# Kernel tuning notes

Measured on AMD Instinct MI355X. Metric: run time of the kernel, lower is better.

The kernel has to match this reference:

```python
import jax, jax.numpy as jnp
import numpy as np

N, E = 50000, 200000
SIZES = [16, 32, 16]
EDIM = 8
EPS = 1e-5


def setup_inputs() -> dict:
    key = jax.random.key(0)
    ks = jax.random.split(key, 16)
    inp = {
        "x": jax.random.normal(ks[0], (N, SIZES[0]), jnp.float32),
        "edge_attr": jax.random.normal(ks[1], (E, EDIM), jnp.float32),
        "edge_index": jax.random.randint(ks[2], (2, E), 0, N, dtype=jnp.int32),
    }
    ki = 3
    for l in range(2):
        fin, fout = SIZES[l], SIZES[l + 1]
        m = fin * fout
        # xavier-ish init matching torch.nn.init.xavier_uniform_ scales
        inp[f"W1_{l}"] = jax.random.normal(ks[ki], (EDIM, m), jnp.float32) / np.float32(np.sqrt(EDIM)); ki += 1
        inp[f"b1_{l}"] = jnp.zeros((m,), jnp.float32)
        inp[f"W2_{l}"] = jax.random.normal(ks[ki], (m, m), jnp.float32) * np.float32(0.01 / np.sqrt(m)); ki += 1
        inp[f"b2_{l}"] = jnp.zeros((m,), jnp.float32)
        inp[f"root_{l}"] = jax.random.normal(ks[ki], (fin, fout), jnp.float32) / np.float32(np.sqrt(fin)); ki += 1
        inp[f"bias_{l}"] = jnp.zeros((fout,), jnp.float32)
        inp[f"gamma_{l}"] = jnp.ones((fout,), jnp.float32)
        inp[f"beta_{l}"] = jnp.zeros((fout,), jnp.float32)
    return inp


def _lrelu(v):
    return jnp.where(v >= 0, v, 0.01 * v)


def _nnconv(x, src, dst, edge_attr, W1, b1, W2, b2, root, bias, fin, fout):
    # edge MLP -> per-edge weight matrix [E, fin, fout]
    h = _lrelu(edge_attr @ W1 + b1) @ W2 + b2
    h = h.reshape(-1, fin, fout)
    # gather source node features, tiny per-edge matmul
    msg = jnp.einsum('ei,eio->eo', x[src], h)  # [E, fout]
    # scatter-mean aggregate at destination nodes
    agg = jax.ops.segment_sum(msg, dst, num_segments=N)
    deg = jax.ops.segment_sum(jnp.ones((msg.shape[0],), msg.dtype), dst, num_segments=N)
    agg = agg / jnp.maximum(deg, 1.0)[:, None]
    return agg + x @ root + bias


def _bn(v, gamma, beta):
    # BatchNorm1d (training mode: batch stats, biased variance)
    mu = v.mean(0)
    var = v.var(0)
    return (v - mu) * jax.lax.rsqrt(var + EPS) * gamma + beta


def reference(x, edge_attr,
              W1_0, b1_0, W2_0, b2_0, root_0, bias_0, gamma_0, beta_0,
              W1_1, b1_1, W2_1, b2_1, root_1, bias_1, gamma_1, beta_1,
              edge_index):
    src, dst = edge_index[0], edge_index[1]
    h = _nnconv(x, src, dst, edge_attr, W1_0, b1_0, W2_0, b2_0, root_0, bias_0, SIZES[0], SIZES[1])
    h = _lrelu(_bn(h, gamma_0, beta_0))
    h = _nnconv(h, src, dst, edge_attr, W1_1, b1_1, W2_1, b2_1, root_1, bias_1, SIZES[1], SIZES[2])
    return _bn(h, gamma_1, beta_1)
```

## Files before the change

### kernel.cpp

```cpp
#include <hip/hip_runtime.h>
#include <hip/hip_bf16.h>

typedef __attribute__((ext_vector_type(4))) float f32x4;
typedef __attribute__((ext_vector_type(8))) short s16x8;
typedef __attribute__((ext_vector_type(4))) int int4v;

#define DEVI __device__ __forceinline__

constexpr int NN = 50000;
constexpr int NE = 200000;
constexpr float BN_EPS = 1e-5f;

DEVI float bfbits2f(unsigned v) { union { unsigned u; float f; } t; t.u = v << 16; return t.f; }
DEVI float lrelu_f(float v) { return v >= 0.f ? v : 0.01f * v; }

__global__ void k_transpose_w2(const float* __restrict__ A0, const float* __restrict__ A1,
                               __hip_bfloat16* __restrict__ T0, __hip_bfloat16* __restrict__ T1) {
  const float* W2 = blockIdx.y ? A1 : A0;
  __hip_bfloat16* W2T = blockIdx.y ? T1 : T0;
  __shared__ float tile[32][33];
  int bx = blockIdx.x % 16, by = blockIdx.x / 16;
  int t = threadIdx.x;
  int r = t / 32, c = t % 32;
  for (int rr = r; rr < 32; rr += 8)
    tile[rr][c] = W2[(size_t)(by * 32 + rr) * 512 + bx * 32 + c];
  __syncthreads();
  for (int rr = r; rr < 32; rr += 8)
    W2T[(size_t)(bx * 32 + rr) * 512 + by * 32 + c] = __float2bfloat16(tile[c][rr]);
}

__global__ void k_transpose_w1(const float* __restrict__ A0, const float* __restrict__ A1,
                               __hip_bfloat16* __restrict__ T0, __hip_bfloat16* __restrict__ T1) {
  const float* W1 = blockIdx.y ? A1 : A0;
  __hip_bfloat16* W1T = blockIdx.y ? T1 : T0;
  int tid = blockIdx.x * 256 + threadIdx.x;
  if (tid < 8 * 512) {
    int k = tid / 512, n = tid % 512;
    W1T[n * 8 + k] = __float2bfloat16(W1[tid]);
  }
}

__global__ void k_count(const int* __restrict__ dst, int* __restrict__ cnt) {
  int e = blockIdx.x * 256 + threadIdx.x;
  if (e < NE) atomicAdd(&cnt[dst[e]], 1);
}

constexpr int SCAN_ELEMS = 1024;
__global__ void k_scan1(const int* __restrict__ cnt, int* __restrict__ base, int* __restrict__ aux, int n) {
  __shared__ int sw[256];
  int b = blockIdx.x, t = threadIdx.x;
  int i0 = b * SCAN_ELEMS + t * 4;
  int v[4]; int s = 0;
  #pragma unroll
  for (int j = 0; j < 4; j++) { int idx = i0 + j; v[j] = (idx < n) ? cnt[idx] : 0; s += v[j]; }
  sw[t] = s; __syncthreads();
  for (int d = 1; d < 256; d <<= 1) {
    int val = (t >= d) ? sw[t - d] : 0;
    __syncthreads();
    sw[t] += val;
    __syncthreads();
  }
  int run = (t > 0) ? sw[t - 1] : 0;
  #pragma unroll
  for (int j = 0; j < 4; j++) { int idx = i0 + j; if (idx < n) base[idx] = run; run += v[j]; }
  if (t == 255) aux[b] = sw[255];
}

__global__ void k_scan2(int* aux, int nb) {
  if (threadIdx.x == 0 && blockIdx.x == 0) {
    int run = 0;
    for (int i = 0; i < nb; i++) { int v = aux[i]; aux[i] = run; run += v; }
  }
}

__global__ void k_scan3(int* __restrict__ base, int* __restrict__ cursor, const int* __restrict__ aux, int n) {
  int i = blockIdx.x * 256 + threadIdx.x;
  if (i < n) { int v = base[i] + aux[i / SCAN_ELEMS]; base[i] = v; cursor[i] = v; }
}

__global__ void k_place(const int* __restrict__ dst, int* __restrict__ cursor, int* __restrict__ perm) {
  int e = blockIdx.x * 256 + threadIdx.x;
  if (e < NE) { int p = atomicAdd(&cursor[dst[e]], 1); perm[p] = e; }
}

template <int FIN, int FOUT>
__global__ __launch_bounds__(256, 2)
void k_edge(const float* __restrict__ x, const float* __restrict__ ea,
            const int* __restrict__ srcI,
            const __hip_bfloat16* __restrict__ W1T, const float* __restrict__ b1,
            const __hip_bfloat16* __restrict__ W2T, const float* __restrict__ b2,
            __hip_bfloat16* __restrict__ msgb)
{
  static_assert(FOUT == 32 || FOUT == 16, "");
  constexpr int TM = 256;
  constexpr int CG = 32;
  constexpr int NCGI = 16;
  constexpr int KH = 256;
  constexpr int NKC = 4;
  constexpr int NOT = FOUT / 16;
  constexpr int XLDS = TM + 8;

  __shared__ __align__(16) char bbuf[2][CG * 512];
  __shared__ __align__(16) char gbuf[4][4096];
  __shared__ __align__(16) __hip_bfloat16 xlt[FIN][XLDS];

  const int tid = threadIdx.x;
  const int lane = tid & 63, w = tid >> 6;
  const int l15 = lane & 15, l4 = lane >> 4;
  const int e0 = blockIdx.x * TM;
  const int rem = min(TM, NE - e0);
  const int wrow0 = w * 64;

  union { s16x8 v; int i4[4]; } earow;
  {
    int er = e0 + min(tid, rem - 1);
    float4 v0 = *(const float4*)(ea + (size_t)er * 8);
    float4 v1 = *(const float4*)(ea + (size_t)er * 8 + 4);
    __hip_bfloat16* p = (__hip_bfloat16*)&earow;
    p[0] = __float2bfloat16(v0.x); p[1] = __float2bfloat16(v0.y);
    p[2] = __float2bfloat16(v0.z); p[3] = __float2bfloat16(v0.w);
    p[4] = __float2bfloat16(v1.x); p[5] = __float2bfloat16(v1.y);
    p[6] = __float2bfloat16(v1.z); p[7] = __float2bfloat16(v1.w);
    int s = srcI[er];
    #pragma unroll
    for (int q = 0; q < FIN / 4; q++) {
      float4 xv4 = *(const float4*)(x + (size_t)s * FIN + q * 4);
      xlt[q * 4 + 0][tid] = __float2bfloat16(xv4.x);
      xlt[q * 4 + 1][tid] = __float2bfloat16(xv4.y);
      xlt[q * 4 + 2][tid] = __float2bfloat16(xv4.z);
      xlt[q * 4 + 3][tid] = __float2bfloat16(xv4.w);
    }
  }

  f32x4 msg[4][NOT];
  #pragma unroll
  for (int rt = 0; rt < 4; rt++)
    #pragma unroll
    for (int ot = 0; ot < NOT; ot++) msg[rt][ot] = (f32x4)(0.f);

  s16x8 af[NKC][4][2];
  const int st_col = tid >> 3, st_s = tid & 7;
  const char* W2Tb = (const char*)W2T;
  char* gme = gbuf[w];
  int4v sr[4];

  for (int sw = 0; sw < 2; ++sw) {
    {
      const char* gp = W2Tb + (size_t)st_col * 1024 + sw * 512;
      #pragma unroll
      for (int j = 0; j < 4; j++) sr[j] = *(const int4v*)(gp + st_s * 16 + j * 128);
    }
    s16x8 afe[4];
    #pragma unroll
    for (int rt = 0; rt < 4; rt++) {
      union { s16x8 v; int i4[4]; } t2;
      #pragma unroll
      for (int q = 0; q < 4; q++) t2.i4[q] = __shfl(earow.i4[q], rt * 16 + l15);
      afe[rt] = (lane < 16) ? t2.v : (s16x8)0;
    }
    #pragma unroll
    for (int h = 0; h < 2; ++h) {
      #pragma unroll
      for (int kc = 0; kc < NKC; kc++) {
        #pragma unroll
        for (int ct = 0; ct < 4; ct++) {
          int c = sw * KH + kc * 64 + ct * 16 + l15;
          s16x8 bw = *(const s16x8*)(W1T + c * 8);
          bw = (lane < 16) ? bw : (s16x8)0;
          float b1v = b1[c];
          #pragma unroll
          for (int rt2 = 0; rt2 < 2; rt2++) {
            f32x4 d = __builtin_amdgcn_mfma_f32_16x16x32_bf16(afe[h * 2 + rt2], bw, (f32x4)(0.f), 0, 0, 0);
            #pragma unroll
            for (int r = 0; r < 4; r++) {
              int rloc = rt2 * 16 + l4 * 4 + r;
              float gv = d[r] + b1v;
              gv = gv >= 0.f ? gv : 0.01f * gv;
              int byt = (rloc * 128 + (ct * 16 + l15) * 2) ^ ((rloc & 7) << 4);
              *(__hip_bfloat16*)(gme + byt) = __float2bfloat16(gv);
            }
          }
        }
        #pragma unroll
        for (int rt2 = 0; rt2 < 2; rt2++)
          #pragma unroll
          for (int ks = 0; ks < 2; ks++) {
            int rloc = rt2 * 16 + l15;
            int byt = (rloc * 128 + (ks * 32 + l4 * 8) * 2) ^ ((rloc & 7) << 4);
            af[kc][h * 2 + rt2][ks] = *(const s16x8*)(gme + byt);
          }
      }
    }
    #pragma unroll
    for (int kc = 0; kc < NKC; kc++)
      #pragma unroll
      for (int rt = 0; rt < 4; rt++)
        #pragma unroll
        for (int ks = 0; ks < 2; ks++)
          asm volatile("" : "+v"(af[kc][rt][ks]));

    #pragma unroll
    for (int j = 0; j < 4; j++)
      *(int4v*)(&bbuf[0][st_col * 512 + (((st_s + 8 * j) ^ (st_col & 7)) << 4)]) = sr[j];
    __syncthreads();

    for (int cgi = 0; cgi < NCGI; ++cgi) {
      if (cgi + 1 < NCGI) {
        const char* gp = W2Tb + (size_t)((cgi + 1) * CG + st_col) * 1024 + sw * 512;
        #pragma unroll
        for (int j = 0; j < 4; j++) sr[j] = *(const int4v*)(gp + st_s * 16 + j * 128);
      }
      const char* bb = bbuf[cgi & 1];
      f32x4 acc[4][2];
      #pragma unroll
      for (int rt = 0; rt < 4; rt++) { acc[rt][0] = (f32x4)(0.f); acc[rt][1] = (f32x4)(0.f); }

      #pragma unroll
      for (int kc = 0; kc < NKC; kc++)
        #pragma unroll
        for (int ct = 0; ct < 2; ct++) {
          const int c = ct * 16 + l15;
          #pragma unroll
          for (int ks = 0; ks < 2; ks++) {
            const int slot = kc * 8 + ks * 4 + l4;
            const s16x8 bw = *(const s16x8*)(bb + c * 512 + ((slot ^ (c & 7)) << 4));
            #pragma unroll
            for (int rt = 0; rt < 4; rt++)
              acc[rt][ct] = __builtin_amdgcn_mfma_f32_16x16x32_bf16(af[kc][rt][ks], bw, acc[rt][ct], 0, 0, 0);
          }
        }

      #pragma unroll
      for (int ct = 0; ct < 2; ct++) {
        float b2v = (sw == 0) ? b2[cgi * CG + ct * 16 + l15] : 0.f;
        const int iv = (FOUT == 32) ? cgi : (cgi * 2 + ct);
        const int ot = (FOUT == 32) ? ct : 0;
        #pragma unroll
        for (int rt = 0; rt < 4; rt++) {
          int rbase = wrow0 + rt * 16 + l4 * 4;
          ushort4 xv = *(const ushort4*)(&xlt[iv][rbase]);
          msg[rt][ot][0] += bfbits2f(xv.x) * (acc[rt][ct][0] + b2v);
          msg[rt][ot][1] += bfbits2f(xv.y) * (acc[rt][ct][1] + b2v);
          msg[rt][ot][2] += bfbits2f(xv.z) * (acc[rt][ct][2] + b2v);
          msg[rt][ot][3] += bfbits2f(xv.w) * (acc[rt][ct][3] + b2v);
        }
      }
      if (cgi + 1 < NCGI) {
        char* bw2 = bbuf[(cgi + 1) & 1];
        #pragma unroll
        for (int j = 0; j < 4; j++)
          *(int4v*)(&bw2[st_col * 512 + (((st_s + 8 * j) ^ (st_col & 7)) << 4)]) = sr[j];
      }
      __syncthreads();
    }
  }

  #pragma unroll
  for (int rt = 0; rt < 4; rt++)
    #pragma unroll
    for (int r = 0; r < 4; r++) {
      int row = wrow0 + rt * 16 + l4 * 4 + r;
      if (row < rem) {
        #pragma unroll
        for (int ot = 0; ot < NOT; ot++)
          msgb[(size_t)(e0 + row) * FOUT + ot * 16 + l15] = __float2bfloat16(msg[rt][ot][r]);
      }
    }
}

template <int FIN, int FOUT>
__global__ void k_node_agg(const __hip_bfloat16* __restrict__ msgb, const int* __restrict__ perm,
                           const int* __restrict__ base,
                           const float* __restrict__ x,
                           const float* __restrict__ root,
                           const float* __restrict__ bias,
                           float* __restrict__ h)
{
  __shared__ float rl[FIN * FOUT];
  constexpr int NPB = 256 / FOUT;
  int t = threadIdx.x;
  for (int i = t; i < FIN * FOUT; i += 256) rl[i] = root[i];
  __syncthreads();
  int n = blockIdx.x * NPB + t / FOUT;
  int o = t % FOUT;
  if (n >= NN) return;
  int s = base[n];
  int e = (n + 1 < NN) ? base[n + 1] : NE;
  float sum = 0.f;
  for (int j = s; j < e; j++)
    sum += __bfloat162float(msgb[(size_t)perm[j] * FOUT + o]);
  float acc = sum / fmaxf((float)(e - s), 1.f) + bias[o];
  #pragma unroll
  for (int i = 0; i < FIN; i++)
    acc += x[(size_t)n * FIN + i] * rl[i * FOUT + o];
  h[(size_t)n * FOUT + o] = acc;
}

template <int FOUT>
__global__ void k_stats(const float* __restrict__ h, float* __restrict__ ssum, float* __restrict__ ssq) {
  constexpr int RPB = 256 / FOUT;
  int t = threadIdx.x;
  int o = t % FOUT, rr = t / FOUT;
  float v = 0.f, v2 = 0.f;
  for (int r = blockIdx.x * RPB + rr; r < NN; r += gridDim.x * RPB) {
    float y = h[(size_t)r * FOUT + o];
    v += y; v2 += y * y;
  }
  #pragma unroll
  for (int d = FOUT; d < 64; d <<= 1) { v += __shfl_xor(v, d); v2 += __shfl_xor(v2, d); }
  __shared__ float sv[4][32], sq[4][32];
  int wv = t >> 6, ln = t & 63;
  if (ln < FOUT) { sv[wv][ln] = v; sq[wv][ln] = v2; }
  __syncthreads();
  if (t < FOUT) {
    float a = 0.f, b = 0.f;
    #pragma unroll
    for (int w2 = 0; w2 < 4; w2++) { a += sv[w2][t]; b += sq[w2][t]; }
    atomicAdd(&ssum[t], a);
    atomicAdd(&ssq[t], b);
  }
}

template <int FOUT, bool LRELU>
__global__ void k_bn(const float* __restrict__ h, const float* __restrict__ ssum,
                     const float* __restrict__ ssq, const float* __restrict__ gamma,
                     const float* __restrict__ beta, float* __restrict__ out)
{
  int idx = blockIdx.x * 256 + threadIdx.x;
  if (idx * 4 >= NN * FOUT) return;
  float4 v = *(const float4*)(h + (size_t)idx * 4);
  float r[4] = {v.x, v.y, v.z, v.w};
  #pragma unroll
  for (int j = 0; j < 4; j++) {
    int o = (idx * 4 + j) % FOUT;
    float mu = ssum[o] * (1.f / NN);
    float var = ssq[o] * (1.f / NN) - mu * mu;
    float sc = rsqrtf(var + BN_EPS) * gamma[o];
    float y = (r[j] - mu) * sc + beta[o];
    if (LRELU) y = lrelu_f(y);
    r[j] = y;
  }
  *(float4*)(out + (size_t)idx * 4) = make_float4(r[0], r[1], r[2], r[3]);
}

extern "C" void kernel_launch(void* const* d_in, const int* in_sizes, int n_in,
                              void* d_out, int out_size, void* d_ws, size_t ws_size,
                              hipStream_t stream)
{
  const float* x0    = (const float*)d_in[0];
  const float* ea    = (const float*)d_in[1];
  const int*   ei    = (const int*)d_in[2];
  const float* W1_0  = (const float*)d_in[3];
  const float* b1_0  = (const float*)d_in[4];
  const float* W2_0  = (const float*)d_in[5];
  const float* b2_0  = (const float*)d_in[6];
  const float* root0 = (const float*)d_in[7];
  const float* bias0 = (const float*)d_in[8];
  const float* gam0  = (const float*)d_in[9];
  const float* bet0  = (const float*)d_in[10];
  const float* W1_1  = (const float*)d_in[11];
  const float* b1_1  = (const float*)d_in[12];
  const float* W2_1  = (const float*)d_in[13];
  const float* b2_1  = (const float*)d_in[14];
  const float* root1 = (const float*)d_in[15];
  const float* bias1 = (const float*)d_in[16];
  const float* gam1  = (const float*)d_in[17];
  const float* bet1  = (const float*)d_in[18];
  const int* srcI = ei;
  const int* dstI = ei + NE;

  char* ws = (char*)d_ws;
  size_t off = 0;
  auto alloc = [&](size_t bytes) { char* p = ws + off; off += (bytes + 255) & ~(size_t)255; return p; };
  int*   cnt   = (int*)alloc(50048 * 4);
  float* ssum0 = (float*)alloc(32 * 4);
  float* ssq0  = (float*)alloc(32 * 4);
  float* ssum1 = (float*)alloc(16 * 4);
  float* ssq1  = (float*)alloc(16 * 4);
  size_t zero_bytes = off;
  int*   base   = (int*)alloc(50048 * 4);
  int*   cursor = (int*)alloc(50048 * 4);
  int*   aux    = (int*)alloc(64 * 4);
  int*   perm   = (int*)alloc((size_t)NE * 4);
  __hip_bfloat16* msgb = (__hip_bfloat16*)alloc((size_t)NE * 32 * 2);
  float* h0 = (float*)alloc((size_t)NN * 32 * 4);
  float* h1 = (float*)alloc((size_t)NN * 16 * 4);
  float* x1 = (float*)alloc((size_t)NN * 32 * 4);
  __hip_bfloat16* W2T0 = (__hip_bfloat16*)alloc(512 * 512 * 2);
  __hip_bfloat16* W2T1 = (__hip_bfloat16*)alloc(512 * 512 * 2);
  __hip_bfloat16* W1T0 = (__hip_bfloat16*)alloc(512 * 8 * 2);
  __hip_bfloat16* W1T1 = (__hip_bfloat16*)alloc(512 * 8 * 2);

  hipMemsetAsync(d_ws, 0, zero_bytes, stream);

  k_transpose_w2<<<dim3(256, 2), 256, 0, stream>>>(W2_0, W2_1, W2T0, W2T1);
  k_transpose_w1<<<dim3(16, 2), 256, 0, stream>>>(W1_0, W1_1, W1T0, W1T1);

  constexpr int NSB = (NN + SCAN_ELEMS - 1) / SCAN_ELEMS;
  k_count<<<(NE + 255) / 256, 256, 0, stream>>>(dstI, cnt);
  k_scan1<<<NSB, 256, 0, stream>>>(cnt, base, aux, NN);
  k_scan2<<<1, 64, 0, stream>>>(aux, NSB);
  k_scan3<<<(NN + 255) / 256, 256, 0, stream>>>(base, cursor, aux, NN);
  k_place<<<(NE + 255) / 256, 256, 0, stream>>>(dstI, cursor, perm);

  constexpr int TM = 256;
  k_edge<16, 32><<<(NE + TM - 1) / TM, 256, 0, stream>>>(x0, ea, srcI, W1T0, b1_0, W2T0, b2_0, msgb);
  k_node_agg<16, 32><<<(NN + 7) / 8, 256, 0, stream>>>(msgb, perm, base, x0, root0, bias0, h0);
  k_stats<32><<<128, 256, 0, stream>>>(h0, ssum0, ssq0);
  k_bn<32, true><<<((NN * 32 / 4) + 255) / 256, 256, 0, stream>>>(h0, ssum0, ssq0, gam0, bet0, x1);

  k_edge<32, 16><<<(NE + TM - 1) / TM, 256, 0, stream>>>(x1, ea, srcI, W1T1, b1_1, W2T1, b2_1, msgb);
  k_node_agg<32, 16><<<(NN + 15) / 16, 256, 0, stream>>>(msgb, perm, base, x1, root1, bias1, h1);
  k_stats<16><<<128, 256, 0, stream>>>(h1, ssum1, ssq1);
  k_bn<16, false><<<((NN * 16 / 4) + 255) / 256, 256, 0, stream>>>(h1, ssum1, ssq1, gam1, bet1, (float*)d_out);
}
```

Baseline: 392.5 us.

## Stream W2 tiles into LDS with direct global-to-LDS loads and fold b2 into accumulator init

Replaces the register-staged W2 tile copy (global load into registers, then LDS store) with global_load_lds direct transfers into the double buffer, with the swizzle applied on the source address. This frees registers and drops the separate LDS write step. It also changes the gbuf swizzle pattern, initialises the MFMA accumulators with b2 instead of adding it afterwards, and raises wave priority around the MFMA loop. The direct loads rely on the per-lane LDS placement matching the existing read swizzle. Nothing in the code waits explicitly for the async loads before the barrier, so correctness depends on the compiler inserting the needed wait.

New measurement: 416.0 us. 6.0% more time.

```diff
diff --git a/kernel.cpp b/kernel.cpp
--- a/kernel.cpp
+++ b/kernel.cpp
@@ -6,6 +6,10 @@
 typedef __attribute__((ext_vector_type(4))) int int4v;
 
 #define DEVI __device__ __forceinline__
+
+#define GLL16(gp, lp) __builtin_amdgcn_global_load_lds( \
+    (const __attribute__((address_space(1))) void*)(gp), \
+    (__attribute__((address_space(3))) void*)(lp), 16, 0, 0)
 
 constexpr int NN = 50000;
 constexpr int NE = 200000;
@@ -139,17 +143,21 @@
     for (int ot = 0; ot < NOT; ot++) msg[rt][ot] = (f32x4)(0.f);
 
   s16x8 af[NKC][4][2];
-  const int st_col = tid >> 3, st_s = tid & 7;
   const char* W2Tb = (const char*)W2T;
   char* gme = gbuf[w];
-  int4v sr[4];
+
+  const int gll_colbase = w * 8 + (lane >> 5);
+  const int gll_sstore = lane & 31;
 
   for (int sw = 0; sw < 2; ++sw) {
-    {
-      const char* gp = W2Tb + (size_t)st_col * 1024 + sw * 512;
-      #pragma unroll
-      for (int j = 0; j < 4; j++) sr[j] = *(const int4v*)(gp + st_s * 16 + j * 128);
-    }
+    #pragma unroll
+    for (int j = 0; j < 4; j++) {
+      int col = gll_colbase + j * 2;
+      int ssrc = gll_sstore ^ (col & 7);
+      const char* gp = W2Tb + (size_t)col * 1024 + sw * 512 + ssrc * 16;
+      GLL16(gp, &bbuf[0][w * 4096 + j * 1024]);
+    }
+
     s16x8 afe[4];
     #pragma unroll
     for (int rt = 0; rt < 4; rt++) {
@@ -176,7 +184,7 @@
               int rloc = rt2 * 16 + l4 * 4 + r;
               float gv = d[r] + b1v;
               gv = gv >= 0.f ? gv : 0.01f * gv;
-              int byt = (rloc * 128 + (ct * 16 + l15) * 2) ^ ((rloc & 7) << 4);
+              int byt = (rloc * 128 + (ct * 16 + l15) * 2) ^ (((rloc >> 2) & 3) << 5);
               *(__hip_bfloat16*)(gme + byt) = __float2bfloat16(gv);
             }
           }
@@ -186,7 +194,7 @@
           #pragma unroll
           for (int ks = 0; ks < 2; ks++) {
             int rloc = rt2 * 16 + l15;
-            int byt = (rloc * 128 + (ks * 32 + l4 * 8) * 2) ^ ((rloc & 7) << 4);
+            int byt = (rloc * 128 + (ks * 32 + l4 * 8) * 2) ^ (((rloc >> 2) & 3) << 5);
             af[kc][h * 2 + rt2][ks] = *(const s16x8*)(gme + byt);
           }
       }
@@ -199,22 +207,33 @@
         for (int ks = 0; ks < 2; ks++)
           asm volatile("" : "+v"(af[kc][rt][ks]));
 
-    #pragma unroll
-    for (int j = 0; j < 4; j++)
-      *(int4v*)(&bbuf[0][st_col * 512 + (((st_s + 8 * j) ^ (st_col & 7)) << 4)]) = sr[j];
     __syncthreads();
 
     for (int cgi = 0; cgi < NCGI; ++cgi) {
       if (cgi + 1 < NCGI) {
-        const char* gp = W2Tb + (size_t)((cgi + 1) * CG + st_col) * 1024 + sw * 512;
-        #pragma unroll
-        for (int j = 0; j < 4; j++) sr[j] = *(const int4v*)(gp + st_s * 16 + j * 128);
+        #pragma unroll
+        for (int j = 0; j < 4; j++) {
+          int col = gll_colbase + j * 2;
+          int ssrc = gll_sstore ^ (col & 7);
+          const char* gp = W2Tb + (size_t)((cgi + 1) * CG + col) * 1024 + sw * 512 + ssrc * 16;
+          GLL16(gp, &bbuf[(cgi + 1) & 1][w * 4096 + j * 1024]);
+        }
       }
       const char* bb = bbuf[cgi & 1];
       f32x4 acc[4][2];
-      #pragma unroll
-      for (int rt = 0; rt < 4; rt++) { acc[rt][0] = (f32x4)(0.f); acc[rt][1] = (f32x4)(0.f); }
-
+      if (sw == 0) {
+        #pragma unroll
+        for (int ct = 0; ct < 2; ct++) {
+          float b2v = b2[cgi * CG + ct * 16 + l15];
+          #pragma unroll
+          for (int rt = 0; rt < 4; rt++) acc[rt][ct] = (f32x4)(b2v);
+        }
+      } else {
+        #pragma unroll
+        for (int rt = 0; rt < 4; rt++) { acc[rt][0] = (f32x4)(0.f); acc[rt][1] = (f32x4)(0.f); }
+      }
+
+      __builtin_amdgcn_s_setprio(1);
       #pragma unroll
       for (int kc = 0; kc < NKC; kc++)
         #pragma unroll
@@ -229,27 +248,21 @@
               acc[rt][ct] = __builtin_amdgcn_mfma_f32_16x16x32_bf16(af[kc][rt][ks], bw, acc[rt][ct], 0, 0, 0);
           }
         }
+      __builtin_amdgcn_s_setprio(0);
 
       #pragma unroll
       for (int ct = 0; ct < 2; ct++) {
-        float b2v = (sw == 0) ? b2[cgi * CG + ct * 16 + l15] : 0.f;
         const int iv = (FOUT == 32) ? cgi : (cgi * 2 + ct);
         const int ot = (FOUT == 32) ? ct : 0;
         #pragma unroll
         for (int rt = 0; rt < 4; rt++) {
           int rbase = wrow0 + rt * 16 + l4 * 4;
           ushort4 xv = *(const ushort4*)(&xlt[iv][rbase]);
-          msg[rt][ot][0] += bfbits2f(xv.x) * (acc[rt][ct][0] + b2v);
-          msg[rt][ot][1] += bfbits2f(xv.y) * (acc[rt][ct][1] + b2v);
-          msg[rt][ot][2] += bfbits2f(xv.z) * (acc[rt][ct][2] + b2v);
-          msg[rt][ot][3] += bfbits2f(xv.w) * (acc[rt][ct][3] + b2v);
+          msg[rt][ot][0] += bfbits2f(xv.x) * acc[rt][ct][0];
+          msg[rt][ot][1] += bfbits2f(xv.y) * acc[rt][ct][1];
+          msg[rt][ot][2] += bfbits2f(xv.z) * acc[rt][ct][2];
+          msg[rt][ot][3] += bfbits2f(xv.w) * acc[rt][ct][3];
         }
-      }
-      if (cgi + 1 < NCGI) {
-        char* bw2 = bbuf[(cgi + 1) & 1];
-        #pragma unroll
-        for (int j = 0; j < 4; j++)
-          *(int4v*)(&bw2[st_col * 512 + (((st_s + 8 * j) ^ (st_col & 7)) << 4)]) = sr[j];
       }
       __syncthreads();
     }
```
